# Kernel tuning notes

Hardware: AMD Instinct MI355X
Metric: run time of the kernel (lower is better)

Reference implementation:

```python
import jax, jax.numpy as jnp
import numpy as np

B, T, N, F = 32, 256, 68, 64
NUM_LAYERS = 3
EPS = 1e-5


def _build_adjacency(n):
    a = np.zeros((n, n), dtype=np.float32)
    i = np.arange(n)
    a[i[1:], i[1:] - 1] = 1.0
    a[i[:-1], i[:-1] + 1] = 1.0
    return jnp.asarray(a)


def setup_inputs() -> dict:
    key = jax.random.key(0)
    ks = jax.random.split(key, 10)
    x = jax.random.normal(ks[0], (B, T, N, 2), dtype=jnp.float32)
    adj = _build_adjacency(N)  # (N, N) tridiagonal buffer (not trainable)
    W_enc = jax.random.normal(ks[1], (2, F), dtype=jnp.float32) * 0.5
    b_enc = jax.random.normal(ks[2], (F,), dtype=jnp.float32) * 0.05
    W_gnn = jax.random.normal(ks[3], (NUM_LAYERS, F, F), dtype=jnp.float32) * (1.0 / np.sqrt(F))
    b_gnn = jax.random.normal(ks[4], (NUM_LAYERS, F), dtype=jnp.float32) * 0.05
    gamma = jnp.ones((NUM_LAYERS, F), dtype=jnp.float32)
    beta = jnp.zeros((NUM_LAYERS, F), dtype=jnp.float32)
    W1 = jax.random.normal(ks[5], (F, 32), dtype=jnp.float32) * (1.0 / np.sqrt(F))
    b1 = jax.random.normal(ks[6], (32,), dtype=jnp.float32) * 0.05
    W2 = jax.random.normal(ks[7], (32, 1), dtype=jnp.float32) * (1.0 / np.sqrt(32))
    b2 = jax.random.normal(ks[8], (1,), dtype=jnp.float32) * 0.05
    return {"landmarks_sequence": x, "adj": adj, "W_enc": W_enc, "b_enc": b_enc,
            "W_gnn": W_gnn, "b_gnn": b_gnn, "gamma": gamma, "beta": beta,
            "W1": W1, "b1": b1, "W2": W2, "b2": b2}


def _layernorm(z, g, b):
    mu = jnp.mean(z, axis=-1, keepdims=True)
    var = jnp.mean(jnp.square(z - mu), axis=-1, keepdims=True)
    return (z - mu) * jax.lax.rsqrt(var + EPS) * g + b


def reference(landmarks_sequence, adj, W_enc, b_enc, W_gnn, b_gnn, gamma, beta, W1, b1, W2, b2):
    # Vectorize the torch per-timestep Python loop: all T timesteps at once.
    # node encoder: (B,T,N,2) -> (B,T,N,F)
    h = landmarks_sequence @ W_enc + b_enc
    for l in range(NUM_LAYERS):
        # neighbor aggregation via tridiagonal adjacency (same math as dense NxN matmul)
        agg = jnp.einsum('nm,btmf->btnf', adj, h)
        z = jax.nn.relu(agg @ W_gnn[l] + b_gnn[l])
        h = _layernorm(z, gamma[l], beta[l]) + h  # residual
    pooled = jnp.mean(h, axis=2)                  # AdaptiveAvgPool1d(1) over nodes -> (B,T,F)
    logits = jax.nn.relu(pooled @ W1 + b1) @ W2 + b2  # (B,T,1)
    return jnp.mean(logits, axis=1).squeeze(-1)       # mean over T, squeeze -> (B,)
```

## Files before the change

### kernel.cpp

```cpp
#include <hip/hip_runtime.h>

#define B_SZ 32
#define T_SZ 256
#define N_NODES 68
#define NLAYERS 3
#define EPS 1e-5f

#define HP 72
#define HROWS 70

typedef _Float16 f16x8 __attribute__((ext_vector_type(8)));
typedef _Float16 f16x4 __attribute__((ext_vector_type(4)));
typedef float    f32x4 __attribute__((ext_vector_type(4)));
typedef int      v2i   __attribute__((ext_vector_type(2)));

__device__ __forceinline__ float red16(float x) {
#if __has_builtin(__builtin_amdgcn_permlane16_swap)
    v2i r = __builtin_amdgcn_permlane16_swap(__float_as_int(x), __float_as_int(x),
                                             false, false);
    return __int_as_float(r[0]) + __int_as_float(r[1]);
#else
    return x + __shfl_xor(x, 16);
#endif
}
__device__ __forceinline__ float red32(float x) {
#if __has_builtin(__builtin_amdgcn_permlane32_swap)
    v2i r = __builtin_amdgcn_permlane32_swap(__float_as_int(x), __float_as_int(x),
                                             false, false);
    return __int_as_float(r[0]) + __int_as_float(r[1]);
#else
    return x + __shfl_xor(x, 32);
#endif
}

__global__ void prep_k(const float* __restrict__ W, const float* __restrict__ W1,
                       const float* __restrict__ gamma, const float* __restrict__ beta,
                       _Float16* __restrict__ Wt, float* __restrict__ W1t,
                       _Float16* __restrict__ gb16, float* __restrict__ out) {
    int idx = blockIdx.x * 256 + threadIdx.x;
    if (idx < 12288) {
        int l = idx >> 12, r = idx & 4095;
        int m = r >> 6, k = r & 63;
        Wt[(l << 12) + (m << 6) + k] = (_Float16)W[(l << 12) + (k << 6) + m];
    } else if (idx < 14336) {
        int r = idx - 12288;
        int j = r >> 6, f = r & 63;
        W1t[r] = W1[f * 32 + j];
    } else if (idx < 14720) {
        int r = idx - 14336;
        gb16[r] = (_Float16)(r < 192 ? gamma[r] : beta[r - 192]);
    } else if (idx < 14752) {
        out[idx - 14720] = 0.f;
    }
}

__global__ __launch_bounds__(256, 2)
void gnn_wave(const float* __restrict__ x,
              const float* __restrict__ W_enc, const float* __restrict__ b_enc,
              const _Float16* __restrict__ Wt, const float* __restrict__ b_gnn,
              const _Float16* __restrict__ gb16,
              const float* __restrict__ W1t, const float* __restrict__ b1,
              const float* __restrict__ W2, const float* __restrict__ b2,
              float* __restrict__ out)
{
    __shared__ _Float16 hsh[4][HROWS * HP];

    const int tid  = threadIdx.x;
    const int lane = tid & 63;
    const int wave = tid >> 6;
    const int l15  = lane & 15;
    const int quad = lane >> 4;

    _Float16* h = hsh[wave];
    const int g = blockIdx.x * 4 + wave;
    const float* xp = x + (size_t)g * (N_NODES * 2);

    if (lane < 36) {
        ((unsigned*)h)[lane] = 0u;
        ((unsigned*)(h + 69 * HP))[lane] = 0u;
    }

    {
        float2 xr[17];
        #pragma unroll
        for (int i = 0; i < 17; ++i)
            xr[i] = *(const float2*)&xp[(i * 4 + quad) * 2];

        const f32x4 we0 = ((const f32x4*)W_enc)[l15];
        const f32x4 we1 = ((const f32x4*)(W_enc + 64))[l15];
        const f32x4 be  = ((const f32x4*)b_enc)[l15];
        #pragma unroll
        for (int i = 0; i < 17; ++i) {
            int n = i * 4 + quad;
            f32x4 hv = xr[i].x * we0 + xr[i].y * we1 + be;
            f16x4 o;
            o[0] = (_Float16)hv[0]; o[1] = (_Float16)hv[1];
            o[2] = (_Float16)hv[2]; o[3] = (_Float16)hv[3];
            *(f16x4*)&h[(n + 1) * HP + l15 * 4] = o;
        }
    }

    #pragma unroll 1
    for (int l = 0; l < NLAYERS; ++l) {
        const _Float16* WtL = Wt + (l << 12);

        __builtin_amdgcn_sched_barrier(0);

        f16x8 a0[4], a1[4];
        f32x4 bgv[4];
        f16x4 gmv[4], bbv[4];
        #pragma unroll
        for (int s = 0; s < 4; ++s) {
            a0[s]  = *(const f16x8*)&WtL[(s * 16 + l15) * 64 + quad * 8];
            a1[s]  = *(const f16x8*)&WtL[(s * 16 + l15) * 64 + 32 + quad * 8];
            bgv[s] = *(const f32x4*)&b_gnn[l * 64 + s * 16 + quad * 4];
            gmv[s] = *(const f16x4*)&gb16[l * 64 + s * 16 + quad * 4];
            bbv[s] = *(const f16x4*)&gb16[192 + l * 64 + s * 16 + quad * 4];
        }

        f16x8 ra0, ra1, rc0, rc1, na0, na1, nc0, nc1;
        {
            const _Float16* hb = h + l15 * HP + quad * 8;
            ra0 = *(const f16x8*)hb;            ra1 = *(const f16x8*)(hb + 32);
            rc0 = *(const f16x8*)(hb + 2 * HP); rc1 = *(const f16x8*)(hb + 2 * HP + 32);
        }

        #pragma unroll
        for (int t = 0; t < 5; ++t) {
            if (t < 4) {
                int n  = (t + 1) * 16 + l15;
                int nc = (t == 3) ? (n > 67 ? 67 : n) : n;
                const _Float16* hb = h + nc * HP + quad * 8;
                na0 = *(const f16x8*)hb;            na1 = *(const f16x8*)(hb + 32);
                nc0 = *(const f16x8*)(hb + 2 * HP); nc1 = *(const f16x8*)(hb + 2 * HP + 32);
            }
            const int rn = t * 16 + l15 + 1;
            f16x4 hv[4];
            #pragma unroll
            for (int s = 0; s < 4; ++s)
                hv[s] = *(const f16x4*)&h[rn * HP + s * 16 + quad * 4];

            f16x8 bc0 = ra0 + rc0;
            f16x8 bc1 = ra1 + rc1;

            f32x4 acc[4];
            #pragma unroll
            for (int s = 0; s < 4; ++s) {
                f32x4 z = {0.f, 0.f, 0.f, 0.f};
                z = __builtin_amdgcn_mfma_f32_16x16x32_f16(a0[s], bc0, z, 0, 0, 0);
                z = __builtin_amdgcn_mfma_f32_16x16x32_f16(a1[s], bc1, z, 0, 0, 0);
                acc[s] = z;
            }

            float Sp[4], Qp[4];
            #pragma unroll
            for (int s = 0; s < 4; ++s) {
                f32x4 zz = acc[s] + bgv[s];
                float s0 = 0.f, q0 = 0.f;
                #pragma unroll
                for (int i = 0; i < 4; ++i) {
                    float zv = fmaxf(zz[i], 0.f);
                    zz[i] = zv; s0 += zv; q0 = fmaf(zv, zv, q0);
                }
                Sp[s] = s0; Qp[s] = q0;
                acc[s] = zz;
            }
            float S = (Sp[0] + Sp[1]) + (Sp[2] + Sp[3]);
            float Q = (Qp[0] + Qp[1]) + (Qp[2] + Qp[3]);
            S = red16(S); Q = red16(Q);
            S = red32(S); Q = red32(Q);
            const float mu = S * (1.f / 64.f);
            const float rs = rsqrtf(fmaf(-mu, mu, Q * (1.f / 64.f)) + EPS);
            const float m2 = -mu * rs;

            __builtin_amdgcn_sched_barrier(0x47F);

            if (t < 4 || l15 < 4) {
                #pragma unroll
                for (int s = 0; s < 4; ++s) {
                    f16x4 th;
                    th[0] = (_Float16)fmaf(acc[s][0], rs, m2);
                    th[1] = (_Float16)fmaf(acc[s][1], rs, m2);
                    th[2] = (_Float16)fmaf(acc[s][2], rs, m2);
                    th[3] = (_Float16)fmaf(acc[s][3], rs, m2);
                    f16x4 r = th * gmv[s] + bbv[s] + hv[s];
                    *(f16x4*)&h[rn * HP + s * 16 + quad * 4] = r;
                }
            }

            ra0 = na0; ra1 = na1; rc0 = nc0; rc1 = nc1;
        }
    }

    __builtin_amdgcn_sched_barrier(0);

    f32x4 pp[4] = {{0.f,0.f,0.f,0.f},{0.f,0.f,0.f,0.f},
                   {0.f,0.f,0.f,0.f},{0.f,0.f,0.f,0.f}};
    #pragma unroll
    for (int i = 0; i < 17; ++i) {
        f16x4 hv = *(const f16x4*)&h[(i * 4 + quad + 1) * HP + l15 * 4];
        f32x4 a = {(float)hv[0], (float)hv[1], (float)hv[2], (float)hv[3]};
        pp[i & 3] += a;
    }
    f32x4 ps = (pp[0] + pp[1]) + (pp[2] + pp[3]);
    #pragma unroll
    for (int i = 0; i < 4; ++i)
        ps[i] = red32(red16(ps[i])) * (1.f / (float)N_NODES);

    __builtin_amdgcn_sched_barrier(0x47F);
    float* scr = (float*)h;
    if (quad == 0) *(f32x4*)&scr[l15 * 4] = ps;
    __builtin_amdgcn_sched_barrier(0x47F);

    {
        const int j = lane & 31, hf = lane >> 5;
        float a = hf ? 0.f : b1[j];
        const float* wrow = W1t + j * 64 + hf * 32;
        const float* pvp  = scr + hf * 32;
        #pragma unroll
        for (int k = 0; k < 8; ++k) {
            f32x4 pw = *(const f32x4*)&wrow[k * 4];
            f32x4 pv = *(const f32x4*)&pvp[k * 4];
            a = fmaf(pv[0], pw[0], a); a = fmaf(pv[1], pw[1], a);
            a = fmaf(pv[2], pw[2], a); a = fmaf(pv[3], pw[3], a);
        }
        float full = red32(a);
        float v = fmaxf(full, 0.f) * W2[j];
        v += __shfl_xor(v, 16);
        v += __shfl_xor(v, 8);
        v += __shfl_xor(v, 4);
        v += __shfl_xor(v, 2);
        v += __shfl_xor(v, 1);
        if (lane == 0)
            atomicAdd(out + (g >> 8), (v + b2[0]) * (1.f / (float)T_SZ));
    }
}

extern "C" void kernel_launch(void* const* d_in, const int* in_sizes, int n_in,
                              void* d_out, int out_size, void* d_ws, size_t ws_size,
                              hipStream_t stream) {
    const float* x     = (const float*)d_in[0];
    const float* W_enc = (const float*)d_in[2];
    const float* b_enc = (const float*)d_in[3];
    const float* W_gnn = (const float*)d_in[4];
    const float* b_gnn = (const float*)d_in[5];
    const float* gamma = (const float*)d_in[6];
    const float* beta  = (const float*)d_in[7];
    const float* W1    = (const float*)d_in[8];
    const float* b1    = (const float*)d_in[9];
    const float* W2    = (const float*)d_in[10];
    const float* b2    = (const float*)d_in[11];
    float* out = (float*)d_out;

    _Float16* Wt   = (_Float16*)d_ws;
    float*    W1t  = (float*)((char*)d_ws + (1 << 15));
    _Float16* gb16 = (_Float16*)((char*)d_ws + 49152);

    prep_k<<<58, 256, 0, stream>>>(W_gnn, W1, gamma, beta, Wt, W1t, gb16, out);

    const int n_graphs = B_SZ * T_SZ;
    gnn_wave<<<n_graphs / 4, 256, 0, stream>>>(x, W_enc, b_enc, Wt, b_gnn,
                                               gb16, W1t, b1, W2, b2, out);
}
```

Baseline: 177.0 us.

## Split each graph across two waves with halo-exchanged node strips

Each graph is now handled by a 128-thread block of two waves, each owning 34 nodes in its own LDS strip. Halo rows are exchanged through double-buffered boundary rows, with __syncthreads after every layer. This halves the per-wave serial MFMA tile loop (3 tiles instead of 5) and shrinks per-wave LDS, which raises parallelism. In exchange it adds block-level barriers, doubles the number of blocks, and uses only a partial last tile of 2 rows out of 16.

```diff
diff --git a/kernel.cpp b/kernel.cpp
--- a/kernel.cpp
+++ b/kernel.cpp
@@ -6,8 +6,8 @@
 #define NLAYERS 3
 #define EPS 1e-5f
 
+#define SROWS 38
 #define HP 72
-#define HROWS 70
 
 typedef _Float16 f16x8 __attribute__((ext_vector_type(8)));
 typedef _Float16 f16x4 __attribute__((ext_vector_type(4)));
@@ -54,7 +54,7 @@
     }
 }
 
-__global__ __launch_bounds__(256, 2)
+__global__ __launch_bounds__(128, 2)
 void gnn_wave(const float* __restrict__ x,
               const float* __restrict__ W_enc, const float* __restrict__ b_enc,
               const _Float16* __restrict__ Wt, const float* __restrict__ b_gnn,
@@ -63,7 +63,8 @@
               const float* __restrict__ W2, const float* __restrict__ b2,
               float* __restrict__ out)
 {
-    __shared__ _Float16 hsh[4][HROWS * HP];
+    __shared__ _Float16 strips[2][SROWS * HP];
+    __shared__ float scr[2][64];
 
     const int tid  = threadIdx.x;
     const int lane = tid & 63;
@@ -71,40 +72,49 @@
     const int l15  = lane & 15;
     const int quad = lane >> 4;
 
-    _Float16* h = hsh[wave];
-    const int g = blockIdx.x * 4 + wave;
+    _Float16* hs = strips[wave];
+    const int base = wave * 34;
+
+    const int g = blockIdx.x;
     const float* xp = x + (size_t)g * (N_NODES * 2);
 
-    if (lane < 36) {
-        ((unsigned*)h)[lane] = 0u;
-        ((unsigned*)(h + 69 * HP))[lane] = 0u;
-    }
+    if (tid < 72)       ((unsigned*)strips[0])[tid] = 0u;
+    else if (tid < 128) ((unsigned*)(strips[1] + 36 * HP))[tid - 72] = 0u;
+    if (tid < 16)       ((unsigned*)(strips[1] + 36 * HP))[56 + tid] = 0u;
 
     {
-        float2 xr[17];
-        #pragma unroll
-        for (int i = 0; i < 17; ++i)
-            xr[i] = *(const float2*)&xp[(i * 4 + quad) * 2];
-
+        float2 xr[9];
+        #pragma unroll
+        for (int i = 0; i < 9; ++i) {
+            int nr = i * 4 + quad;
+            int nc = nr < 34 ? nr : 33;
+            xr[i] = *(const float2*)&xp[(base + nc) * 2];
+        }
         const f32x4 we0 = ((const f32x4*)W_enc)[l15];
         const f32x4 we1 = ((const f32x4*)(W_enc + 64))[l15];
         const f32x4 be  = ((const f32x4*)b_enc)[l15];
         #pragma unroll
-        for (int i = 0; i < 17; ++i) {
-            int n = i * 4 + quad;
+        for (int i = 0; i < 9; ++i) {
+            int nr = i * 4 + quad;
             f32x4 hv = xr[i].x * we0 + xr[i].y * we1 + be;
             f16x4 o;
             o[0] = (_Float16)hv[0]; o[1] = (_Float16)hv[1];
             o[2] = (_Float16)hv[2]; o[3] = (_Float16)hv[3];
-            *(f16x4*)&h[(n + 1) * HP + l15 * 4] = o;
-        }
-    }
+            if (nr < 34)
+                *(f16x4*)&hs[(2 + nr) * HP + l15 * 4] = o;
+            if (wave == 0 && i == 8 && quad == 1)
+                *(f16x4*)&strips[1][0 * HP + l15 * 4] = o;
+            if (wave == 1 && i == 0 && quad == 0)
+                *(f16x4*)&strips[0][36 * HP + l15 * 4] = o;
+        }
+    }
+    __syncthreads();
 
     #pragma unroll 1
     for (int l = 0; l < NLAYERS; ++l) {
         const _Float16* WtL = Wt + (l << 12);
-
-        __builtin_amdgcn_sched_barrier(0);
+        const int par  = l & 1;
+        const int parn = par ^ 1;
 
         f16x8 a0[4], a1[4];
         f32x4 bgv[4];
@@ -118,27 +128,28 @@
             bbv[s] = *(const f16x4*)&gb16[192 + l * 64 + s * 16 + quad * 4];
         }
 
+        auto read_raw = [&](int t, f16x8& x0, f16x8& x1, f16x8& y0, f16x8& y1) {
+            const int j  = (t < 2) ? (t * 16 + l15) : (l15 == 0 ? 32 : 33);
+            const int rA = (j == 0)  ? par        : (1 + j);
+            const int rB = (j == 33) ? (36 + par) : (3 + j);
+            const _Float16* pa = hs + rA * HP + quad * 8;
+            const _Float16* pb = hs + rB * HP + quad * 8;
+            x0 = *(const f16x8*)pa; x1 = *(const f16x8*)(pa + 32);
+            y0 = *(const f16x8*)pb; y1 = *(const f16x8*)(pb + 32);
+        };
+
         f16x8 ra0, ra1, rc0, rc1, na0, na1, nc0, nc1;
-        {
-            const _Float16* hb = h + l15 * HP + quad * 8;
-            ra0 = *(const f16x8*)hb;            ra1 = *(const f16x8*)(hb + 32);
-            rc0 = *(const f16x8*)(hb + 2 * HP); rc1 = *(const f16x8*)(hb + 2 * HP + 32);
-        }
-
-        #pragma unroll
-        for (int t = 0; t < 5; ++t) {
-            if (t < 4) {
-                int n  = (t + 1) * 16 + l15;
-                int nc = (t == 3) ? (n > 67 ? 67 : n) : n;
-                const _Float16* hb = h + nc * HP + quad * 8;
-                na0 = *(const f16x8*)hb;            na1 = *(const f16x8*)(hb + 32);
-                nc0 = *(const f16x8*)(hb + 2 * HP); nc1 = *(const f16x8*)(hb + 2 * HP + 32);
-            }
-            const int rn = t * 16 + l15 + 1;
+        read_raw(0, ra0, ra1, rc0, rc1);
+
+        #pragma unroll
+        for (int t = 0; t < 3; ++t) {
+            if (t < 2) read_raw(t + 1, na0, na1, nc0, nc1);
+            const int j  = (t < 2) ? (t * 16 + l15) : (l15 == 0 ? 32 : 33);
+            const int rO = 2 + j;
             f16x4 hv[4];
             #pragma unroll
             for (int s = 0; s < 4; ++s)
-                hv[s] = *(const f16x4*)&h[rn * HP + s * 16 + quad * 4];
+                hv[s] = *(const f16x4*)&hs[rO * HP + s * 16 + quad * 4];
 
             f16x8 bc0 = ra0 + rc0;
             f16x8 bc1 = ra1 + rc1;
@@ -175,7 +186,7 @@
 
             __builtin_amdgcn_sched_barrier(0x47F);
 
-            if (t < 4 || l15 < 4) {
+            if (t < 2 || l15 < 2) {
                 #pragma unroll
                 for (int s = 0; s < 4; ++s) {
                     f16x4 th;
@@ -184,43 +195,47 @@
                     th[2] = (_Float16)fmaf(acc[s][2], rs, m2);
                     th[3] = (_Float16)fmaf(acc[s][3], rs, m2);
                     f16x4 r = th * gmv[s] + bbv[s] + hv[s];
-                    *(f16x4*)&h[rn * HP + s * 16 + quad * 4] = r;
+                    *(f16x4*)&hs[rO * HP + s * 16 + quad * 4] = r;
+                    if (wave == 0 && t == 2 && l15 == 1)
+                        *(f16x4*)&strips[1][parn * HP + s * 16 + quad * 4] = r;
+                    if (wave == 1 && t == 0 && l15 == 0)
+                        *(f16x4*)&strips[0][(36 + parn) * HP + s * 16 + quad * 4] = r;
                 }
             }
 
             ra0 = na0; ra1 = na1; rc0 = nc0; rc1 = nc1;
         }
-    }
-
-    __builtin_amdgcn_sched_barrier(0);
+        __syncthreads();
+    }
 
     f32x4 pp[4] = {{0.f,0.f,0.f,0.f},{0.f,0.f,0.f,0.f},
                    {0.f,0.f,0.f,0.f},{0.f,0.f,0.f,0.f}};
     #pragma unroll
-    for (int i = 0; i < 17; ++i) {
-        f16x4 hv = *(const f16x4*)&h[(i * 4 + quad + 1) * HP + l15 * 4];
-        f32x4 a = {(float)hv[0], (float)hv[1], (float)hv[2], (float)hv[3]};
-        pp[i & 3] += a;
+    for (int i = 0; i < 9; ++i) {
+        int nr = i * 4 + quad;
+        if (nr < 34) {
+            f16x4 hv = *(const f16x4*)&hs[(2 + nr) * HP + l15 * 4];
+            f32x4 a = {(float)hv[0], (float)hv[1], (float)hv[2], (float)hv[3]};
+            pp[i & 3] += a;
+        }
     }
     f32x4 ps = (pp[0] + pp[1]) + (pp[2] + pp[3]);
     #pragma unroll
     for (int i = 0; i < 4; ++i)
-        ps[i] = red32(red16(ps[i])) * (1.f / (float)N_NODES);
-
-    __builtin_amdgcn_sched_barrier(0x47F);
-    float* scr = (float*)h;
-    if (quad == 0) *(f32x4*)&scr[l15 * 4] = ps;
-    __builtin_amdgcn_sched_barrier(0x47F);
-
-    {
+        ps[i] = red32(red16(ps[i]));
+    if (quad == 0) *(f32x4*)&scr[wave][l15 * 4] = ps;
+    __syncthreads();
+
+    if (wave == 0) {
         const int j = lane & 31, hf = lane >> 5;
         float a = hf ? 0.f : b1[j];
         const float* wrow = W1t + j * 64 + hf * 32;
-        const float* pvp  = scr + hf * 32;
         #pragma unroll
         for (int k = 0; k < 8; ++k) {
             f32x4 pw = *(const f32x4*)&wrow[k * 4];
-            f32x4 pv = *(const f32x4*)&pvp[k * 4];
+            f32x4 p0 = *(const f32x4*)&scr[0][hf * 32 + k * 4];
+            f32x4 p1 = *(const f32x4*)&scr[1][hf * 32 + k * 4];
+            f32x4 pv = (p0 + p1) * (1.f / (float)N_NODES);
             a = fmaf(pv[0], pw[0], a); a = fmaf(pv[1], pw[1], a);
             a = fmaf(pv[2], pw[2], a); a = fmaf(pv[3], pw[3], a);
         }
@@ -259,6 +274,6 @@
     prep_k<<<58, 256, 0, stream>>>(W_gnn, W1, gamma, beta, Wt, W1t, gb16, out);
 
     const int n_graphs = B_SZ * T_SZ;
-    gnn_wave<<<n_graphs / 4, 256, 0, stream>>>(x, W_enc, b_enc, Wt, b_gnn,
-                                               gb16, W1t, b1, W2, b2, out);
-}
+    gnn_wave<<<n_graphs, 128, 0, stream>>>(x, W_enc, b_enc, Wt, b_gnn,
+                                           gb16, W1t, b1, W2, b2, out);
+}
```

Measured after the change: 191.5 us. 8.1% more time.
